# Performance work log

Hardware: AMD Instinct MI355X
Metric: run time of the kernel (lower is better)

## Reference

```python
import jax, jax.numpy as jnp
import numpy as np

BATCH = 256
DIMS = [256, 512, 256, 128]  # input_dim + hidden_dims + [output_dim]
GRID = 5


def _kan_layer(x, w, s, b, g):
    # x: (B, in); w: (out, in, G); s: (out, in); b: (out,); g: (G,)
    xn = jnp.tanh(x)
    # distances: (B, out, in, G)
    d = jnp.abs(xn[:, None, :, None] - g[None, None, None, :])
    basis = jnp.exp(-d * s[None, :, :, None])
    # sum over grid then in_features, fused into one einsum
    return jnp.einsum('boig,oig->bo', basis, w) + b


def setup_inputs() -> dict:
    key = jax.random.key(0)
    ks = jax.random.split(key, 8)
    inp = {'x': jax.random.normal(ks[0], (BATCH, DIMS[0]), dtype=jnp.float32)}
    for i in range(3):
        din, dout = DIMS[i], DIMS[i + 1]
        k1, k2 = jax.random.split(ks[i + 1])
        inp[f'w{i}'] = jax.random.normal(k1, (dout, din, GRID), dtype=jnp.float32)
        inp[f's{i}'] = jax.random.normal(k2, (dout, din), dtype=jnp.float32)
        inp[f'b{i}'] = jnp.zeros((dout,), dtype=jnp.float32)
        inp[f'g{i}'] = jnp.linspace(-1.0, 1.0, GRID, dtype=jnp.float32)
    return inp


def reference(x, w0, s0, b0, g0, w1, s1, b1, g1, w2, s2, b2, g2):
    h = _kan_layer(x, w0, s0, b0, g0)
    h = jax.nn.relu(h)
    h = _kan_layer(h, w1, s1, b1, g1)
    h = jax.nn.relu(h)
    h = _kan_layer(h, w2, s2, b2, g2)
    return jnp.tanh(h)
```

## Files before the change

kernel.cpp:

```cpp
#include <hip/hip_runtime.h>
#include <math.h>

#define BATCH 256
#define D0 256
#define D1 512
#define D2 256
#define D3 128

__device__ float g_xnT0[D0 * BATCH];
__device__ float g_xnT1[D1 * BATCH];
__device__ float g_xnT2[D2 * BATCH];

template <int L> __device__ __forceinline__ float* xnT_ptr() {
    if constexpr (L == 0) return g_xnT0;
    else if constexpr (L == 1) return g_xnT1;
    else return g_xnT2;
}

__device__ __forceinline__ float tanh_f32_cr(float x) {
    return (float)tanh((double)x);
}

__global__ void prep_tanhT(const float* __restrict__ x) {
    int i = threadIdx.x;
    int b = blockIdx.x;
    g_xnT0[i * BATCH + b] = tanh_f32_cr(x[b * D0 + i]);
}

template <int L, int IN, int OUT, bool FINAL>
__global__ __launch_bounds__(64, 2) void kan_layer(
    const float* __restrict__ w, const float* __restrict__ s,
    const float* __restrict__ bias, float* __restrict__ outf)
{
#pragma clang fp contract(off)
    const int o = blockIdx.x;
    const int b = blockIdx.y * 64 + threadIdx.x;
    const float* __restrict__ xnT = xnT_ptr<L>();
    const float* __restrict__ wr = w + (size_t)o * IN * 5;
    const float* __restrict__ sr = s + (size_t)o * IN;
    constexpr int K = IN * 5;

    float vacc[4] = {0.f, 0.f, 0.f, 0.f};

#pragma unroll 1
    for (int blk = 0; blk < K; blk += 80) {
        const int ibase = blk / 5;
        float xnv[16];
#pragma unroll
        for (int ii = 0; ii < 16; ++ii)
            xnv[ii] = xnT[(ibase + ii) * BATCH + b];

#pragma unroll
        for (int q = 0; q < 5; ++q) {
            float p[16];
#pragma unroll
            for (int c = 0; c < 4; ++c) {
                double uu[4], pp[4];
                int ni[4];
#pragma unroll
                for (int t = 0; t < 4; ++t) {
                    const int u = q * 16 + c * 4 + t;
                    const int i = u / 5;
                    const int gi = u % 5;
                    const float gv = 0.5f * (float)gi - 1.0f;
                    const float d = fabsf(xnv[i] - gv);
                    const float m = -(d * sr[ibase + i]);
                    const double tt = (double)m * 1.4426950408889634;
                    const double nn = rint(tt);
                    ni[t] = (int)nn;
                    uu[t] = (tt - nn) * 0.6931471805599453;
                }
#pragma unroll
                for (int t = 0; t < 4; ++t) pp[t] = fma(1.0 / 40320.0, uu[t], 1.0 / 5040.0);
#pragma unroll
                for (int t = 0; t < 4; ++t) pp[t] = fma(pp[t], uu[t], 1.0 / 720.0);
#pragma unroll
                for (int t = 0; t < 4; ++t) pp[t] = fma(pp[t], uu[t], 1.0 / 120.0);
#pragma unroll
                for (int t = 0; t < 4; ++t) pp[t] = fma(pp[t], uu[t], 1.0 / 24.0);
#pragma unroll
                for (int t = 0; t < 4; ++t) pp[t] = fma(pp[t], uu[t], 1.0 / 6.0);
#pragma unroll
                for (int t = 0; t < 4; ++t) pp[t] = fma(pp[t], uu[t], 0.5);
#pragma unroll
                for (int t = 0; t < 4; ++t) pp[t] = fma(pp[t], uu[t], 1.0);
#pragma unroll
                for (int t = 0; t < 4; ++t) pp[t] = fma(pp[t], uu[t], 1.0);
#pragma unroll
                for (int t = 0; t < 4; ++t)
                    p[c * 4 + t] = ldexpf((float)pp[t], ni[t]) * wr[blk + q * 16 + c * 4 + t];
            }
#pragma unroll
            for (int l = 0; l < 4; ++l) {
                float a = vacc[l];
                a = p[12 + l] + a;
                a = p[8 + l] + a;
                a = p[4 + l] + a;
                vacc[l] = p[0 + l] + a;
            }
        }
    }

    float h = (vacc[0] + vacc[1]) + (vacc[2] + vacc[3]);
    h = h + bias[o];

    if constexpr (FINAL) {
        outf[b * OUT + o] = tanh_f32_cr(h);
    } else {
        xnT_ptr<L + 1>()[o * BATCH + b] = tanh_f32_cr(fmaxf(h, 0.0f));
    }
}

extern "C" void kernel_launch(void* const* d_in, const int* in_sizes, int n_in,
                              void* d_out, int out_size, void* d_ws, size_t ws_size,
                              hipStream_t stream)
{
    const float* x  = (const float*)d_in[0];
    const float* w0 = (const float*)d_in[1];
    const float* s0 = (const float*)d_in[2];
    const float* b0 = (const float*)d_in[3];
    const float* w1 = (const float*)d_in[5];
    const float* s1 = (const float*)d_in[6];
    const float* b1 = (const float*)d_in[7];
    const float* w2 = (const float*)d_in[9];
    const float* s2 = (const float*)d_in[10];
    const float* b2 = (const float*)d_in[11];
    float* out = (float*)d_out;

    prep_tanhT<<<dim3(BATCH), dim3(D0), 0, stream>>>(x);

    kan_layer<0, D0, D1, false><<<dim3(D1, BATCH / 64), dim3(64), 0, stream>>>(w0, s0, b0, nullptr);
    kan_layer<1, D1, D2, false><<<dim3(D2, BATCH / 64), dim3(64), 0, stream>>>(w1, s1, b1, nullptr);
    kan_layer<2, D2, D3, true ><<<dim3(D3, BATCH / 64), dim3(64), 0, stream>>>(w2, s2, b2, out);
}
```

Before: 374.2 us.

## Split each batch row's reduction across four lanes with shuffle combine

Each block now uses 256 threads, where four consecutive lanes share one batch element and each lane computes a strided quarter of the IN*5 basis terms. Partial sums are combined with two xor shuffles, and lane 0 writes the result. The aim is four times more threads in flight to hide the long double-precision exp polynomial latency. The cost is that each lane now loads xn and s per term instead of reusing them from registers, and the summation order changes slightly.

```diff
diff --git a/kernel.cpp b/kernel.cpp
--- a/kernel.cpp
+++ b/kernel.cpp
@@ -28,86 +28,96 @@
 }
 
 template <int L, int IN, int OUT, bool FINAL>
-__global__ __launch_bounds__(64, 2) void kan_layer(
+__global__ __launch_bounds__(256, 4) void kan_layer(
     const float* __restrict__ w, const float* __restrict__ s,
     const float* __restrict__ bias, float* __restrict__ outf)
 {
 #pragma clang fp contract(off)
     const int o = blockIdx.x;
-    const int b = blockIdx.y * 64 + threadIdx.x;
+    const int tid = threadIdx.x;
+    const int l = tid & 3;
+    const int b = blockIdx.y * 64 + (tid >> 2);
     const float* __restrict__ xnT = xnT_ptr<L>();
     const float* __restrict__ wr = w + (size_t)o * IN * 5;
     const float* __restrict__ sr = s + (size_t)o * IN;
     constexpr int K = IN * 5;
 
-    float vacc[4] = {0.f, 0.f, 0.f, 0.f};
+    float gvc[5];
+    int   iac[5];
+#pragma unroll
+    for (int c = 0; c < 5; ++c) {
+        const int sum = c + l;
+        const int carry = (sum >= 5) ? 1 : 0;
+        iac[c] = carry;
+        gvc[c] = 0.5f * (float)(sum - 5 * carry) - 1.0f;
+    }
+
+    float acc = 0.f;
 
 #pragma unroll 1
     for (int blk = 0; blk < K; blk += 80) {
         const int ibase = blk / 5;
-        float xnv[16];
-#pragma unroll
-        for (int ii = 0; ii < 16; ++ii)
-            xnv[ii] = xnT[(ibase + ii) * BATCH + b];
-
 #pragma unroll
         for (int q = 0; q < 5; ++q) {
-            float p[16];
+            float mm[4];
+            float wv[4];
 #pragma unroll
-            for (int c = 0; c < 4; ++c) {
-                double uu[4], pp[4];
-                int ni[4];
+            for (int j = 0; j < 4; ++j) {
+                const int C = q * 16 + 4 * j;
+                const int c = C % 5;
+                const int i = ibase + C / 5 + iac[c];
+                const float xn = xnT[i * BATCH + b];
+                const float sv = sr[i];
+                const float d = fabsf(xn - gvc[c]);
+                mm[j] = -(d * sv);
+                wv[j] = wr[blk + C + l];
+            }
+            double uu[4], pp[4];
+            int ni[4];
 #pragma unroll
-                for (int t = 0; t < 4; ++t) {
-                    const int u = q * 16 + c * 4 + t;
-                    const int i = u / 5;
-                    const int gi = u % 5;
-                    const float gv = 0.5f * (float)gi - 1.0f;
-                    const float d = fabsf(xnv[i] - gv);
-                    const float m = -(d * sr[ibase + i]);
-                    const double tt = (double)m * 1.4426950408889634;
-                    const double nn = rint(tt);
-                    ni[t] = (int)nn;
-                    uu[t] = (tt - nn) * 0.6931471805599453;
-                }
-#pragma unroll
-                for (int t = 0; t < 4; ++t) pp[t] = fma(1.0 / 40320.0, uu[t], 1.0 / 5040.0);
-#pragma unroll
-                for (int t = 0; t < 4; ++t) pp[t] = fma(pp[t], uu[t], 1.0 / 720.0);
-#pragma unroll
-                for (int t = 0; t < 4; ++t) pp[t] = fma(pp[t], uu[t], 1.0 / 120.0);
-#pragma unroll
-                for (int t = 0; t < 4; ++t) pp[t] = fma(pp[t], uu[t], 1.0 / 24.0);
-#pragma unroll
-                for (int t = 0; t < 4; ++t) pp[t] = fma(pp[t], uu[t], 1.0 / 6.0);
-#pragma unroll
-                for (int t = 0; t < 4; ++t) pp[t] = fma(pp[t], uu[t], 0.5);
-#pragma unroll
-                for (int t = 0; t < 4; ++t) pp[t] = fma(pp[t], uu[t], 1.0);
-#pragma unroll
-                for (int t = 0; t < 4; ++t) pp[t] = fma(pp[t], uu[t], 1.0);
-#pragma unroll
-                for (int t = 0; t < 4; ++t)
-                    p[c * 4 + t] = ldexpf((float)pp[t], ni[t]) * wr[blk + q * 16 + c * 4 + t];
+            for (int j = 0; j < 4; ++j) {
+                const double tt = (double)mm[j] * 1.4426950408889634;
+                const double nn = rint(tt);
+                ni[j] = (int)nn;
+                uu[j] = (tt - nn) * 0.6931471805599453;
             }
 #pragma unroll
-            for (int l = 0; l < 4; ++l) {
-                float a = vacc[l];
-                a = p[12 + l] + a;
-                a = p[8 + l] + a;
-                a = p[4 + l] + a;
-                vacc[l] = p[0 + l] + a;
-            }
+            for (int j = 0; j < 4; ++j) pp[j] = fma(1.0 / 40320.0, uu[j], 1.0 / 5040.0);
+#pragma unroll
+            for (int j = 0; j < 4; ++j) pp[j] = fma(pp[j], uu[j], 1.0 / 720.0);
+#pragma unroll
+            for (int j = 0; j < 4; ++j) pp[j] = fma(pp[j], uu[j], 1.0 / 120.0);
+#pragma unroll
+            for (int j = 0; j < 4; ++j) pp[j] = fma(pp[j], uu[j], 1.0 / 24.0);
+#pragma unroll
+            for (int j = 0; j < 4; ++j) pp[j] = fma(pp[j], uu[j], 1.0 / 6.0);
+#pragma unroll
+            for (int j = 0; j < 4; ++j) pp[j] = fma(pp[j], uu[j], 0.5);
+#pragma unroll
+            for (int j = 0; j < 4; ++j) pp[j] = fma(pp[j], uu[j], 1.0);
+#pragma unroll
+            for (int j = 0; j < 4; ++j) pp[j] = fma(pp[j], uu[j], 1.0);
+            float p[4];
+#pragma unroll
+            for (int j = 0; j < 4; ++j)
+                p[j] = ldexpf((float)pp[j], ni[j]) * wv[j];
+            acc = p[3] + acc;
+            acc = p[2] + acc;
+            acc = p[1] + acc;
+            acc = p[0] + acc;
         }
     }
 
-    float h = (vacc[0] + vacc[1]) + (vacc[2] + vacc[3]);
+    float v01 = acc + __shfl_xor(acc, 1);
+    float h   = v01 + __shfl_xor(v01, 2);
     h = h + bias[o];
 
-    if constexpr (FINAL) {
-        outf[b * OUT + o] = tanh_f32_cr(h);
-    } else {
-        xnT_ptr<L + 1>()[o * BATCH + b] = tanh_f32_cr(fmaxf(h, 0.0f));
+    if (l == 0) {
+        if constexpr (FINAL) {
+            outf[b * OUT + o] = tanh_f32_cr(h);
+        } else {
+            xnT_ptr<L + 1>()[o * BATCH + b] = tanh_f32_cr(fmaxf(h, 0.0f));
+        }
     }
 }
 
@@ -129,7 +139,7 @@
 
     prep_tanhT<<<dim3(BATCH), dim3(D0), 0, stream>>>(x);
 
-    kan_layer<0, D0, D1, false><<<dim3(D1, BATCH / 64), dim3(64), 0, stream>>>(w0, s0, b0, nullptr);
-    kan_layer<1, D1, D2, false><<<dim3(D2, BATCH / 64), dim3(64), 0, stream>>>(w1, s1, b1, nullptr);
-    kan_layer<2, D2, D3, true ><<<dim3(D3, BATCH / 64), dim3(64), 0, stream>>>(w2, s2, b2, out);
+    kan_layer<0, D0, D1, false><<<dim3(D1, BATCH / 64), dim3(256), 0, stream>>>(w0, s0, b0, nullptr);
+    kan_layer<1, D1, D2, false><<<dim3(D2, BATCH / 64), dim3(256), 0, stream>>>(w1, s1, b1, nullptr);
+    kan_layer<2, D2, D3, true ><<<dim3(D3, BATCH / 64), dim3(256), 0, stream>>>(w2, s2, b2, out);
 }
```

After: 485.1 us. +29.6%, slower.
